# Kernel optimization log

Measured on AMD Instinct MI355X. Metric: run time of the kernel, lower is better.

## Reference

```python
import jax, jax.numpy as jnp
import numpy as np

EMB_DIM = 768
HEAD = 12
HEAD_DIM = EMB_DIM // HEAD


def setup_inputs() -> dict:
    key = jax.random.key(0)
    ks = jax.random.split(key, 6)
    B, N, D = 8, 1024, EMB_DIM
    s = 1.0 / np.sqrt(D)
    return {
        "z": jax.random.normal(ks[0], (B, N, D), dtype=jnp.float32),
        "w_q": jax.random.normal(ks[1], (D, D), dtype=jnp.float32) * s,
        "w_k": jax.random.normal(ks[2], (D, D), dtype=jnp.float32) * s,
        "w_v": jax.random.normal(ks[3], (D, D), dtype=jnp.float32) * s,
        "w_o": jax.random.normal(ks[4], (D, D), dtype=jnp.float32) * s,
        "b_o": jax.random.normal(ks[5], (D,), dtype=jnp.float32) * 0.01,
    }


def reference(z, w_q, w_k, w_v, w_o, b_o):
    B, N, D = z.shape
    sqrt_dh = jnp.asarray(HEAD_DIM, z.dtype) ** 0.5
    # project and split heads: [B, H, N, Dh]
    def heads(x, w):
        return (x @ w.T).reshape(B, N, HEAD, HEAD_DIM).transpose(0, 2, 1, 3)
    q = heads(z, w_q)
    k = heads(z, w_k)
    v = heads(z, w_v)
    dots = jnp.einsum("bhqd,bhkd->bhqk", q, k) / sqrt_dh
    attn = jax.nn.softmax(dots, axis=-1)  # dropout p=0 -> identity
    out = jnp.einsum("bhqk,bhkd->bhqd", attn, v)
    out = out.transpose(0, 2, 1, 3).reshape(B, N, D)
    return out @ w_o.T + b_o
```

## Files before the change

kernel.cpp:

```cpp
#include <hip/hip_runtime.h>
#include <hip/hip_bf16.h>
#include <stdint.h>

typedef unsigned short u16;
typedef __attribute__((ext_vector_type(8))) short bf16x8;
typedef __attribute__((ext_vector_type(4))) float f32x4;

__device__ __forceinline__ u16 f2bf(float f) {
    union { float f; unsigned int i; } c; c.f = f;
    unsigned int x = c.i;
    return (u16)((x + 0x7FFFu + ((x >> 16) & 1u)) >> 16);
}
__device__ __forceinline__ u16 f2bf_fast(float f) {
    union { float f; unsigned int i; } c; c.f = f;
    return (u16)((c.i + 0x8000u) >> 16);
}

__device__ __forceinline__ void glds16(const u16* g, u16* l) {
    __builtin_amdgcn_global_load_lds(
        (const __attribute__((address_space(1))) void*)g,
        (__attribute__((address_space(3))) void*)l, 16, 0, 0);
}

__device__ __forceinline__ void bar() { asm volatile("s_barrier" ::: "memory"); }
template <int N> __device__ __forceinline__ void waitv() {
    if constexpr (N == 0)      asm volatile("s_waitcnt vmcnt(0)" ::: "memory");
    else if constexpr (N == 2) asm volatile("s_waitcnt vmcnt(2)" ::: "memory");
    else if constexpr (N == 3) asm volatile("s_waitcnt vmcnt(3)" ::: "memory");
    else if constexpr (N == 4) asm volatile("s_waitcnt vmcnt(4)" ::: "memory");
    else if constexpr (N == 8) asm volatile("s_waitcnt vmcnt(8)" ::: "memory");
}

__global__ __launch_bounds__(256) void convert_all(
    const float* __restrict__ z, const float* __restrict__ wq,
    const float* __restrict__ wk, const float* __restrict__ wv,
    const float* __restrict__ wo,
    u16* __restrict__ zb, u16* __restrict__ wqb, u16* __restrict__ wkb,
    u16* __restrict__ wvb, u16* __restrict__ wob)
{
    int g = blockIdx.x * 256 + threadIdx.x;
    const float* s; u16* d;
    if (g < 786432)       { s = z;  d = zb;  }
    else if (g < 860160)  { s = wq; d = wqb; g -= 786432; }
    else if (g < 933888)  { s = wk; d = wkb; g -= 860160; }
    else if (g < 1007616) { s = wv; d = wvb; g -= 933888; }
    else                  { s = wo; d = wob; g -= 1007616; }
    float4 a = *(const float4*)(s + (size_t)g * 8);
    float4 b = *(const float4*)(s + (size_t)g * 8 + 4);
    u16 t[8] = {f2bf(a.x), f2bf(a.y), f2bf(a.z), f2bf(a.w),
                f2bf(b.x), f2bf(b.y), f2bf(b.z), f2bf(b.w)};
    *(uint4*)(d + (size_t)g * 8) = *(const uint4*)t;
}

__global__ __launch_bounds__(256) void qkv_gemm(
    const u16* __restrict__ zb, const u16* __restrict__ wqb,
    const u16* __restrict__ wkb, const u16* __restrict__ wvb,
    u16* __restrict__ qkb, u16* __restrict__ vt)
{
    __shared__ __align__(16) u16 As[8192], Bs[8192];
    const int d = blockIdx.x;
    const int n0 = (d >> 6) * 128, m0 = (d & 63) * 128;
    const u16* Bp;
    if (n0 < 768)       Bp = wqb + (size_t)n0 * 768;
    else if (n0 < 1536) Bp = wkb + (size_t)(n0 - 768) * 768;
    else                Bp = wvb + (size_t)(n0 - 1536) * 768;

    const int t = threadIdx.x;
    const int w = t >> 6, lane = t & 63, quad = lane >> 4, lc = lane & 15;
    const int wm = w >> 1, wn = w & 1;
    const int swz = (lc >> 1) & 3;

    const u16* pa[2]; const u16* pb[2]; int la[2], lb[2];
    #pragma unroll
    for (int j = 0; j < 2; j++) {
        const int c = j * 256 + t;
        const int row = c >> 2;
        const int kq = (c & 3) ^ ((row >> 1) & 3);
        pa[j] = &zb[(size_t)(m0 + row) * 768 + kq * 8];
        pb[j] = &Bp[(size_t)row * 768 + kq * 8];
        la[j] = lb[j] = (j * 256 + w * 64) * 8;
    }

    glds16(pa[0], As + la[0]);  glds16(pa[1], As + la[1]);
    glds16(pb[0], Bs + lb[0]);  glds16(pb[1], Bs + lb[1]);
    glds16(pa[0] + 32, As + 4096 + la[0]);  glds16(pa[1] + 32, As + 4096 + la[1]);
    glds16(pb[0] + 32, Bs + 4096 + lb[0]);  glds16(pb[1] + 32, Bs + 4096 + lb[1]);

    f32x4 acc[4][4] = {};
    int buf = 0;
    for (int bk = 0; bk < 24; bk++) {
        if (bk + 1 < 24) waitv<4>(); else waitv<0>();
        bar();
        bf16x8 af[4], bfr[4];
        #pragma unroll
        for (int i = 0; i < 4; i++) {
            const int row = 64 * wm + 16 * i + lc;
            af[i] = *(const bf16x8*)&As[buf * 4096 + (row * 4 + (quad ^ swz)) * 8];
        }
        #pragma unroll
        for (int j = 0; j < 4; j++) {
            const int row = 64 * wn + 16 * j + lc;
            bfr[j] = *(const bf16x8*)&Bs[buf * 4096 + (row * 4 + (quad ^ swz)) * 8];
        }
        #pragma unroll
        for (int i = 0; i < 4; i++)
            #pragma unroll
            for (int j = 0; j < 4; j++)
                acc[i][j] = __builtin_amdgcn_mfma_f32_16x16x32_bf16(af[i], bfr[j], acc[i][j], 0, 0, 0);
        bar();
        if (bk + 2 < 24) {
            const int k2 = (bk + 2) * 32;
            glds16(pa[0] + k2, As + buf * 4096 + la[0]);
            glds16(pa[1] + k2, As + buf * 4096 + la[1]);
            glds16(pb[0] + k2, Bs + buf * 4096 + lb[0]);
            glds16(pb[1] + k2, Bs + buf * 4096 + lb[1]);
        }
        buf ^= 1;
    }

    if (n0 < 1536) {
        #pragma unroll
        for (int i = 0; i < 4; i++)
            #pragma unroll
            for (int j = 0; j < 4; j++) {
                const int col = n0 + 64 * wn + 16 * j + lc;
                #pragma unroll
                for (int r = 0; r < 4; r++) {
                    const int row = m0 + 64 * wm + 16 * i + quad * 4 + r;
                    qkb[(size_t)row * 1536 + col] = f2bf_fast(acc[i][j][r]);
                }
            }
    } else {
        #pragma unroll
        for (int i = 0; i < 4; i++)
            #pragma unroll
            for (int j = 0; j < 4; j++) {
                const int c = (n0 - 1536) + 64 * wn + 16 * j + lc;
                const int h = c >> 6, dd = c & 63;
                const int tok0 = m0 + 64 * wm + 16 * i + quad * 4;
                const int b = tok0 >> 10, n = tok0 & 1023;
                ushort4 pk = { f2bf_fast(acc[i][j][0]), f2bf_fast(acc[i][j][1]),
                               f2bf_fast(acc[i][j][2]), f2bf_fast(acc[i][j][3]) };
                *(ushort4*)&vt[(((size_t)(b * 12 + h)) * 64 + dd) * 1024 + n] = pk;
            }
    }
}

__global__ __launch_bounds__(256) void oproj_gemm(
    const u16* __restrict__ ob, const u16* __restrict__ wob,
    const float* __restrict__ bo, float* __restrict__ out)
{
    __shared__ __align__(16) u16 As[4096], Bs[8192];
    const int d = blockIdx.x;
    const int n0 = (d >> 7) * 128, m0 = (d & 127) * 64;

    const int t = threadIdx.x;
    const int w = t >> 6, lane = t & 63, quad = lane >> 4, lc = lane & 15;
    const int wm = w >> 1, wn = w & 1;
    const int swz = (lc >> 1) & 3;

    const int arow = t >> 2;
    const int akq = (t & 3) ^ ((arow >> 1) & 3);
    const u16* pa = &ob[(size_t)(m0 + arow) * 768 + akq * 8];
    const int la = (w * 64) * 8;
    const u16* pb[2]; int lb[2];
    #pragma unroll
    for (int j = 0; j < 2; j++) {
        const int c = j * 256 + t;
        const int row = c >> 2;
        const int kq = (c & 3) ^ ((row >> 1) & 3);
        pb[j] = &wob[(size_t)(n0 + row) * 768 + kq * 8];
        lb[j] = (j * 256 + w * 64) * 8;
    }

    glds16(pa, As + la);
    glds16(pb[0], Bs + lb[0]);  glds16(pb[1], Bs + lb[1]);
    glds16(pa + 32, As + 2048 + la);
    glds16(pb[0] + 32, Bs + 4096 + lb[0]);  glds16(pb[1] + 32, Bs + 4096 + lb[1]);

    f32x4 acc[2][4] = {};
    int buf = 0;
    for (int bk = 0; bk < 24; bk++) {
        if (bk + 1 < 24) waitv<3>(); else waitv<0>();
        bar();
        bf16x8 af[2], bfr[4];
        #pragma unroll
        for (int i = 0; i < 2; i++) {
            const int row = 32 * wm + 16 * i + lc;
            af[i] = *(const bf16x8*)&As[buf * 2048 + (row * 4 + (quad ^ swz)) * 8];
        }
        #pragma unroll
        for (int j = 0; j < 4; j++) {
            const int row = 64 * wn + 16 * j + lc;
            bfr[j] = *(const bf16x8*)&Bs[buf * 4096 + (row * 4 + (quad ^ swz)) * 8];
        }
        #pragma unroll
        for (int i = 0; i < 2; i++)
            #pragma unroll
            for (int j = 0; j < 4; j++)
                acc[i][j] = __builtin_amdgcn_mfma_f32_16x16x32_bf16(af[i], bfr[j], acc[i][j], 0, 0, 0);
        bar();
        if (bk + 2 < 24) {
            const int k2 = (bk + 2) * 32;
            glds16(pa + k2, As + buf * 2048 + la);
            glds16(pb[0] + k2, Bs + buf * 4096 + lb[0]);
            glds16(pb[1] + k2, Bs + buf * 4096 + lb[1]);
        }
        buf ^= 1;
    }

    #pragma unroll
    for (int i = 0; i < 2; i++)
        #pragma unroll
        for (int j = 0; j < 4; j++) {
            const int col = n0 + 64 * wn + 16 * j + lc;
            const float bv = bo[col];
            #pragma unroll
            for (int r = 0; r < 4; r++) {
                const int row = m0 + 32 * wm + 16 * i + quad * 4 + r;
                out[(size_t)row * 768 + col] = acc[i][j][r] + bv;
            }
        }
}

__global__ __launch_bounds__(256, 4) void attn_kernel(
    const u16* __restrict__ qkb, const u16* __restrict__ vt,
    u16* __restrict__ obuf)
{
    const int b = blockIdx.x / 12, h = blockIdx.x % 12;
    const int q0 = blockIdx.y * 128;
    const int t = threadIdx.x;
    const int w = t >> 6, lane = t & 63, quad = lane >> 4, lc = lane & 15;

    const u16* Qp  = qkb + (size_t)b * 1024 * 1536 + h * 64;
    const u16* Kp  = Qp + 768;
    const u16* Vtp = vt + ((size_t)(b * 12 + h)) * 64 * 1024;

    __shared__ __align__(16) u16 Ks[2][4096];
    __shared__ __align__(16) u16 Vts[4096];
    __shared__ __align__(16) u16 Ps[8192];

    const u16* kp[2]; int kl[2];
    #pragma unroll
    for (int j = 0; j < 2; j++) {
        const int c = j * 256 + t;
        const int row = c >> 3;
        const int kq = (c & 7) ^ ((row >> 1) & 7);
        kp[j] = Kp + (size_t)row * 1536 + kq * 8;
        kl[j] = (j * 256 + w * 64) * 8;
    }
    const u16* vp[2]; u16* vl[2];
    #pragma unroll
    for (int s2 = 0; s2 < 2; s2++) {
        const int s = 2 * w + s2;
        const int c = s * 64 + lane;
        const int dd = c >> 3, kq = (c & 7) ^ (dd & 7);
        vp[s2] = Vtp + (size_t)dd * 1024 + kq * 8;
        vl[s2] = &Vts[s * 512];
    }

    bf16x8 qf[2][2];
    #pragma unroll
    for (int rg = 0; rg < 2; rg++)
        #pragma unroll
        for (int kk = 0; kk < 2; kk++)
            qf[rg][kk] = *(const bf16x8*)&Qp[(size_t)(q0 + 32 * w + 16 * rg + lc) * 1536
                                             + kk * 32 + quad * 8];

    f32x4 oacc[2][4] = {};
    float lsum[2][4] = {};

    const float cs = 0.18033688011112042f;
    const int swk = (lc >> 1) & 7;
    const int pR0 = 32 * w;

    waitv<0>();
    glds16(kp[0], &Ks[0][0] + kl[0]);
    glds16(kp[1], &Ks[0][0] + kl[1]);

    for (int kt = 0; kt < 16; kt++) {
        const int kb = kt * 64;
        bar();
        glds16(vp[0] + kb, vl[0]);
        glds16(vp[1] + kb, vl[1]);
        if (kt + 1 < 16) {
            const size_t kb1 = (size_t)(kt + 1) * 64 * 1536;
            u16* kd = &Ks[(kt + 1) & 1][0];
            glds16(kp[0] + kb1, kd + kl[0]);
            glds16(kp[1] + kb1, kd + kl[1]);
            waitv<4>();
        } else {
            waitv<2>();
        }
        bar();

        const u16* Kc = &Ks[kt & 1][0];
        f32x4 sacc[2][4] = {};
        #pragma unroll
        for (int j = 0; j < 4; j++) {
            const int nrow = 16 * j + lc;
            bf16x8 kf0 = *(const bf16x8*)&Kc[(nrow * 8 + (quad ^ swk)) * 8];
            bf16x8 kf1 = *(const bf16x8*)&Kc[(nrow * 8 + ((4 + quad) ^ swk)) * 8];
            #pragma unroll
            for (int rg = 0; rg < 2; rg++) {
                sacc[rg][j] = __builtin_amdgcn_mfma_f32_16x16x32_bf16(qf[rg][0], kf0, sacc[rg][j], 0, 0, 0);
                sacc[rg][j] = __builtin_amdgcn_mfma_f32_16x16x32_bf16(qf[rg][1], kf1, sacc[rg][j], 0, 0, 0);
            }
        }
        if (kt + 1 < 16) waitv<2>();
        else             waitv<0>();
        bar();

        #pragma unroll
        for (int rg = 0; rg < 2; rg++) {
            const int Rb = pR0 + 16 * rg + quad * 4;
            #pragma unroll
            for (int j = 0; j < 4; j++)
                #pragma unroll
                for (int r = 0; r < 4; r++) {
                    float p = __builtin_amdgcn_exp2f(sacc[rg][j][r] * cs);
                    lsum[rg][r] += p;
                    const int R = Rb + r;
                    const int slot = (2 * j + (lc >> 3)) ^ ((R >> 1) & 7);
                    Ps[R * 64 + slot * 8 + (lc & 7)] = f2bf_fast(p);
                }
        }

        #pragma unroll
        for (int ks = 0; ks < 2; ks++) {
            bf16x8 pa[2];
            #pragma unroll
            for (int rg = 0; rg < 2; rg++) {
                const int Rp = pR0 + 16 * rg + lc;
                pa[rg] = *(const bf16x8*)&Ps[Rp * 64 + (((ks * 4 + quad) ^ ((Rp >> 1) & 7)) << 3)];
            }
            #pragma unroll
            for (int jd = 0; jd < 4; jd++) {
                const int dd = 16 * jd + lc;
                bf16x8 vb = *(const bf16x8*)&Vts[(dd * 8 + ((ks * 4 + quad) ^ (dd & 7))) * 8];
                #pragma unroll
                for (int rg = 0; rg < 2; rg++)
                    oacc[rg][jd] = __builtin_amdgcn_mfma_f32_16x16x32_bf16(pa[rg], vb, oacc[rg][jd], 0, 0, 0);
            }
        }
    }

    #pragma unroll
    for (int off = 1; off < 16; off <<= 1)
        #pragma unroll
        for (int rg = 0; rg < 2; rg++)
            #pragma unroll
            for (int r = 0; r < 4; r++)
                lsum[rg][r] += __shfl_xor(lsum[rg][r], off, 64);

    float invl[2][4];
    #pragma unroll
    for (int rg = 0; rg < 2; rg++)
        #pragma unroll
        for (int r = 0; r < 4; r++) invl[rg][r] = __builtin_amdgcn_rcpf(lsum[rg][r]);
    #pragma unroll
    for (int rg = 0; rg < 2; rg++)
        #pragma unroll
        for (int jd = 0; jd < 4; jd++)
            #pragma unroll
            for (int r = 0; r < 4; r++) {
                const int row = q0 + 32 * w + 16 * rg + quad * 4 + r;
                const int col = h * 64 + 16 * jd + lc;
                obuf[((size_t)b * 1024 + row) * 768 + col] = f2bf_fast(oacc[rg][jd][r] * invl[rg][r]);
            }
}

extern "C" void kernel_launch(void* const* d_in, const int* in_sizes, int n_in,
                              void* d_out, int out_size, void* d_ws, size_t ws_size,
                              hipStream_t stream) {
    const float* z  = (const float*)d_in[0];
    const float* wq = (const float*)d_in[1];
    const float* wk = (const float*)d_in[2];
    const float* wv = (const float*)d_in[3];
    const float* wo = (const float*)d_in[4];
    const float* bo = (const float*)d_in[5];

    u16* ws16 = (u16*)d_ws;
    u16* zb   = ws16;
    u16* wqb  = zb  + 6291456;
    u16* wkb  = wqb + 589824;
    u16* wvb  = wkb + 589824;
    u16* wob  = wvb + 589824;
    u16* vt   = wob + 589824;
    u16* qkb  = (u16*)d_out;
    u16* obuf = zb;
    float* out = (float*)d_out;

    convert_all<<<4224, 256, 0, stream>>>(z, wq, wk, wv, wo, zb, wqb, wkb, wvb, wob);
    qkv_gemm<<<1152, 256, 0, stream>>>(zb, wqb, wkb, wvb, qkb, vt);
    attn_kernel<<<dim3(96, 8), 256, 0, stream>>>(qkb, vt, obuf);
    oproj_gemm<<<768, 256, 0, stream>>>(obuf, wob, bo, out);
}
```

Measured before the change: 191.6 us.

## Keep attention P in registers via transposed scores and drop LDS staging

```diff
diff --git a/kernel.cpp b/kernel.cpp
--- a/kernel.cpp
+++ b/kernel.cpp
@@ -4,6 +4,7 @@
 
 typedef unsigned short u16;
 typedef __attribute__((ext_vector_type(8))) short bf16x8;
+typedef __attribute__((ext_vector_type(4))) short bf16x4;
 typedef __attribute__((ext_vector_type(4))) float f32x4;
 
 __device__ __forceinline__ u16 f2bf(float f) {
@@ -14,6 +15,16 @@
 __device__ __forceinline__ u16 f2bf_fast(float f) {
     union { float f; unsigned int i; } c; c.f = f;
     return (u16)((c.i + 0x8000u) >> 16);
+}
+
+__device__ __forceinline__ f32x4 mfma16(bf16x4 a, bf16x4 b, f32x4 c) {
+#if __has_builtin(__builtin_amdgcn_mfma_f32_16x16x16bf16_1k)
+    return __builtin_amdgcn_mfma_f32_16x16x16bf16_1k(a, b, c, 0, 0, 0);
+#else
+    asm volatile("v_mfma_f32_16x16x16_bf16 %0, %1, %2, %0"
+                 : "+v"(c) : "v"(a), "v"(b));
+    return c;
+#endif
 }
 
 __device__ __forceinline__ void glds16(const u16* g, u16* l) {
@@ -223,7 +234,7 @@
         }
 }
 
-__global__ __launch_bounds__(256, 4) void attn_kernel(
+__global__ __launch_bounds__(256, 2) void attn_kernel(
     const u16* __restrict__ qkb, const u16* __restrict__ vt,
     u16* __restrict__ obuf)
 {
@@ -236,29 +247,6 @@
     const u16* Kp  = Qp + 768;
     const u16* Vtp = vt + ((size_t)(b * 12 + h)) * 64 * 1024;
 
-    __shared__ __align__(16) u16 Ks[2][4096];
-    __shared__ __align__(16) u16 Vts[4096];
-    __shared__ __align__(16) u16 Ps[8192];
-
-    const u16* kp[2]; int kl[2];
-    #pragma unroll
-    for (int j = 0; j < 2; j++) {
-        const int c = j * 256 + t;
-        const int row = c >> 3;
-        const int kq = (c & 7) ^ ((row >> 1) & 7);
-        kp[j] = Kp + (size_t)row * 1536 + kq * 8;
-        kl[j] = (j * 256 + w * 64) * 8;
-    }
-    const u16* vp[2]; u16* vl[2];
-    #pragma unroll
-    for (int s2 = 0; s2 < 2; s2++) {
-        const int s = 2 * w + s2;
-        const int c = s * 64 + lane;
-        const int dd = c >> 3, kq = (c & 7) ^ (dd & 7);
-        vp[s2] = Vtp + (size_t)dd * 1024 + kq * 8;
-        vl[s2] = &Vts[s * 512];
-    }
-
     bf16x8 qf[2][2];
     #pragma unroll
     for (int rg = 0; rg < 2; rg++)
@@ -267,107 +255,88 @@
             qf[rg][kk] = *(const bf16x8*)&Qp[(size_t)(q0 + 32 * w + 16 * rg + lc) * 1536
                                              + kk * 32 + quad * 8];
 
-    f32x4 oacc[2][4] = {};
-    float lsum[2][4] = {};
-
+    f32x4 oaccT[2][4] = {};
+    float lsum[2] = {0.0f, 0.0f};
     const float cs = 0.18033688011112042f;
-    const int swk = (lc >> 1) & 7;
-    const int pR0 = 32 * w;
-
-    waitv<0>();
-    glds16(kp[0], &Ks[0][0] + kl[0]);
-    glds16(kp[1], &Ks[0][0] + kl[1]);
 
     for (int kt = 0; kt < 16; kt++) {
         const int kb = kt * 64;
-        bar();
-        glds16(vp[0] + kb, vl[0]);
-        glds16(vp[1] + kb, vl[1]);
-        if (kt + 1 < 16) {
-            const size_t kb1 = (size_t)(kt + 1) * 64 * 1536;
-            u16* kd = &Ks[(kt + 1) & 1][0];
-            glds16(kp[0] + kb1, kd + kl[0]);
-            glds16(kp[1] + kb1, kd + kl[1]);
-            waitv<4>();
-        } else {
-            waitv<2>();
-        }
-        bar();
-
-        const u16* Kc = &Ks[kt & 1][0];
-        f32x4 sacc[2][4] = {};
-        #pragma unroll
-        for (int j = 0; j < 4; j++) {
-            const int nrow = 16 * j + lc;
-            bf16x8 kf0 = *(const bf16x8*)&Kc[(nrow * 8 + (quad ^ swk)) * 8];
-            bf16x8 kf1 = *(const bf16x8*)&Kc[(nrow * 8 + ((4 + quad) ^ swk)) * 8];
+
+        bf16x8 kf[4][2];
+        #pragma unroll
+        for (int jk = 0; jk < 4; jk++) {
+            const u16* kr = &Kp[(size_t)(kb + 16 * jk + lc) * 1536 + quad * 8];
+            kf[jk][0] = *(const bf16x8*)kr;
+            kf[jk][1] = *(const bf16x8*)(kr + 32);
+        }
+        bf16x4 vf[4][4];
+        #pragma unroll
+        for (int jd = 0; jd < 4; jd++) {
+            const u16* vr = &Vtp[(size_t)(16 * jd + lc) * 1024 + kb + 4 * quad];
+            #pragma unroll
+            for (int jk = 0; jk < 4; jk++)
+                vf[jk][jd] = *(const bf16x4*)(vr + 16 * jk);
+        }
+
+        f32x4 st[2][4] = {};
+        #pragma unroll
+        for (int jk = 0; jk < 4; jk++)
             #pragma unroll
             for (int rg = 0; rg < 2; rg++) {
-                sacc[rg][j] = __builtin_amdgcn_mfma_f32_16x16x32_bf16(qf[rg][0], kf0, sacc[rg][j], 0, 0, 0);
-                sacc[rg][j] = __builtin_amdgcn_mfma_f32_16x16x32_bf16(qf[rg][1], kf1, sacc[rg][j], 0, 0, 0);
-            }
-        }
-        if (kt + 1 < 16) waitv<2>();
-        else             waitv<0>();
-        bar();
-
-        #pragma unroll
-        for (int rg = 0; rg < 2; rg++) {
-            const int Rb = pR0 + 16 * rg + quad * 4;
-            #pragma unroll
-            for (int j = 0; j < 4; j++)
+                st[rg][jk] = __builtin_amdgcn_mfma_f32_16x16x32_bf16(kf[jk][0], qf[rg][0], st[rg][jk], 0, 0, 0);
+                st[rg][jk] = __builtin_amdgcn_mfma_f32_16x16x32_bf16(kf[jk][1], qf[rg][1], st[rg][jk], 0, 0, 0);
+            }
+
+        bf16x4 pf[2][4];
+        #pragma unroll
+        for (int rg = 0; rg < 2; rg++)
+            #pragma unroll
+            for (int jk = 0; jk < 4; jk++) {
+                float p0 = __builtin_amdgcn_exp2f(st[rg][jk][0] * cs);
+                float p1 = __builtin_amdgcn_exp2f(st[rg][jk][1] * cs);
+                float p2 = __builtin_amdgcn_exp2f(st[rg][jk][2] * cs);
+                float p3 = __builtin_amdgcn_exp2f(st[rg][jk][3] * cs);
+                lsum[rg] += (p0 + p1) + (p2 + p3);
+                bf16x4 pk;
+                pk[0] = (short)f2bf_fast(p0);
+                pk[1] = (short)f2bf_fast(p1);
+                pk[2] = (short)f2bf_fast(p2);
+                pk[3] = (short)f2bf_fast(p3);
+                pf[rg][jk] = pk;
+            }
+
+        #pragma unroll
+        for (int jk = 0; jk < 4; jk++)
+            #pragma unroll
+            for (int rg = 0; rg < 2; rg++)
                 #pragma unroll
-                for (int r = 0; r < 4; r++) {
-                    float p = __builtin_amdgcn_exp2f(sacc[rg][j][r] * cs);
-                    lsum[rg][r] += p;
-                    const int R = Rb + r;
-                    const int slot = (2 * j + (lc >> 3)) ^ ((R >> 1) & 7);
-                    Ps[R * 64 + slot * 8 + (lc & 7)] = f2bf_fast(p);
-                }
-        }
-
-        #pragma unroll
-        for (int ks = 0; ks < 2; ks++) {
-            bf16x8 pa[2];
-            #pragma unroll
-            for (int rg = 0; rg < 2; rg++) {
-                const int Rp = pR0 + 16 * rg + lc;
-                pa[rg] = *(const bf16x8*)&Ps[Rp * 64 + (((ks * 4 + quad) ^ ((Rp >> 1) & 7)) << 3)];
-            }
-            #pragma unroll
-            for (int jd = 0; jd < 4; jd++) {
-                const int dd = 16 * jd + lc;
-                bf16x8 vb = *(const bf16x8*)&Vts[(dd * 8 + ((ks * 4 + quad) ^ (dd & 7))) * 8];
-                #pragma unroll
-                for (int rg = 0; rg < 2; rg++)
-                    oacc[rg][jd] = __builtin_amdgcn_mfma_f32_16x16x32_bf16(pa[rg], vb, oacc[rg][jd], 0, 0, 0);
-            }
-        }
-    }
-
-    #pragma unroll
-    for (int off = 1; off < 16; off <<= 1)
-        #pragma unroll
-        for (int rg = 0; rg < 2; rg++)
-            #pragma unroll
-            for (int r = 0; r < 4; r++)
-                lsum[rg][r] += __shfl_xor(lsum[rg][r], off, 64);
-
-    float invl[2][4];
-    #pragma unroll
-    for (int rg = 0; rg < 2; rg++)
-        #pragma unroll
-        for (int r = 0; r < 4; r++) invl[rg][r] = __builtin_amdgcn_rcpf(lsum[rg][r]);
-    #pragma unroll
-    for (int rg = 0; rg < 2; rg++)
+                for (int jd = 0; jd < 4; jd++)
+                    oaccT[rg][jd] = mfma16(pf[rg][jk], vf[jk][jd], oaccT[rg][jd]);
+    }
+
+    float invl[2];
+    #pragma unroll
+    for (int rg = 0; rg < 2; rg++) {
+        lsum[rg] += __shfl_xor(lsum[rg], 16, 64);
+        lsum[rg] += __shfl_xor(lsum[rg], 32, 64);
+        invl[rg] = __builtin_amdgcn_rcpf(lsum[rg]);
+    }
+
+    #pragma unroll
+    for (int rg = 0; rg < 2; rg++) {
+        float invq[4];
+        #pragma unroll
+        for (int r = 0; r < 4; r++)
+            invq[r] = __shfl(invl[rg], (lane & 48) + 4 * quad + r, 64);
         #pragma unroll
         for (int jd = 0; jd < 4; jd++)
             #pragma unroll
             for (int r = 0; r < 4; r++) {
-                const int row = q0 + 32 * w + 16 * rg + quad * 4 + r;
+                const int row = q0 + 32 * w + 16 * rg + 4 * quad + r;
                 const int col = h * 64 + 16 * jd + lc;
-                obuf[((size_t)b * 1024 + row) * 768 + col] = f2bf_fast(oacc[rg][jd][r] * invl[rg][r]);
-            }
+                obuf[((size_t)b * 1024 + row) * 768 + col] = f2bf_fast(oaccT[rg][jd][r] * invq[r]);
+            }
+    }
 }
 
 extern "C" void kernel_launch(void* const* d_in, const int* in_sizes, int n_in,
```

After: 279.8 us. 46.0% more time.
